# Kernel optimization log

Measured on AMD Instinct MI355X. Metric: run time of the kernel, lower is better.

The kernel has to match this reference:

```python
import jax, jax.numpy as jnp
import numpy as np

NEG_SLOPE = 0.2

def gatv2_layer(x, src, dst, Wl, bl, Wr, br, att, bias, N, concat):
    # Wl/Wr: [F_in, H*C]; att: [H, C]
    H, C = att.shape
    xl = (x @ Wl + bl).reshape(-1, H, C)  # source transform [N,H,C]
    xr = (x @ Wr + br).reshape(-1, H, C)  # target transform [N,H,C]
    e = jax.nn.leaky_relu(xl[src] + xr[dst], NEG_SLOPE)          # [E,H,C]
    logits = jnp.einsum('ehc,hc->eh', e, att)                    # [E,H]
    m = jax.ops.segment_max(logits, dst, num_segments=N)         # [N,H]
    p = jnp.exp(logits - m[dst])
    s = jax.ops.segment_sum(p, dst, num_segments=N)              # [N,H]
    alpha = p / s[dst]                                           # [E,H] softmax per dst
    out = jax.ops.segment_sum(alpha[:, :, None] * xl[src], dst, num_segments=N)  # [N,H,C]
    out = out.reshape(N, H * C) if concat else out.mean(axis=1)
    return out + bias


def setup_inputs() -> dict:
    key = jax.random.key(0)
    N, E, F_in = 50000, 500000, 58
    ks = jax.random.split(key, 16)
    s = 0.1
    inp = {
        'x': jax.random.normal(ks[0], (N, F_in), jnp.float32),
        'edge_index': jax.random.randint(ks[1], (2, E), 0, N, jnp.int64),
        'Wl1': jax.random.normal(ks[2], (F_in, 256), jnp.float32) * s,
        'bl1': jnp.zeros((256,), jnp.float32),
        'Wr1': jax.random.normal(ks[3], (F_in, 256), jnp.float32) * s,
        'br1': jnp.zeros((256,), jnp.float32),
        'att1': jax.random.normal(ks[4], (4, 64), jnp.float32) * s,
        'bias1': jnp.zeros((256,), jnp.float32),
        'Wl2': jax.random.normal(ks[5], (256, 256), jnp.float32) * s,
        'bl2': jnp.zeros((256,), jnp.float32),
        'Wr2': jax.random.normal(ks[6], (256, 256), jnp.float32) * s,
        'br2': jnp.zeros((256,), jnp.float32),
        'att2': jax.random.normal(ks[7], (4, 64), jnp.float32) * s,
        'bias2': jnp.zeros((256,), jnp.float32),
        'Wl3': jax.random.normal(ks[8], (256, 6), jnp.float32) * s,
        'bl3': jnp.zeros((6,), jnp.float32),
        'Wr3': jax.random.normal(ks[9], (256, 6), jnp.float32) * s,
        'br3': jnp.zeros((6,), jnp.float32),
        'att3': jax.random.normal(ks[10], (6, 1), jnp.float32) * s,
        'bias3': jnp.zeros((1,), jnp.float32),
    }
    return inp


def reference(x, edge_index, Wl1, bl1, Wr1, br1, att1, bias1,
              Wl2, bl2, Wr2, br2, att2, bias2,
              Wl3, bl3, Wr3, br3, att3, bias3):
    N = x.shape[0]
    loop = jnp.arange(N, dtype=edge_index.dtype)
    src = jnp.concatenate([edge_index[0], loop])  # self-loops (PyG default)
    dst = jnp.concatenate([edge_index[1], loop])
    h = jax.nn.elu(gatv2_layer(x, src, dst, Wl1, bl1, Wr1, br1, att1, bias1, N, True))
    h = jax.nn.elu(gatv2_layer(h, src, dst, Wl2, bl2, Wr2, br2, att2, bias2, N, True))
    out = gatv2_layer(h, src, dst, Wl3, bl3, Wr3, br3, att3, bias3, N, False)
    return out  # [N, 1]
```

## Files before the change

### kernel.cpp

```cpp
#include <hip/hip_runtime.h>
#include <math.h>

#define NEG_SLOPE 0.2f
#define LOG2E 1.4426950408889634f

typedef __attribute__((ext_vector_type(2))) _Float16 h2;
typedef __attribute__((ext_vector_type(4))) _Float16 h4;
typedef __attribute__((ext_vector_type(8))) _Float16 f16x8;
typedef __attribute__((ext_vector_type(4))) float f32x4;

typedef const __attribute__((address_space(1))) unsigned int* gu32p;
typedef __attribute__((address_space(3))) unsigned int* lu32p;

#define GLD16(g, l) __builtin_amdgcn_global_load_lds((gu32p)(g), (lu32p)(l), 16, 0, 0)

template<int CTRL>
__device__ __forceinline__ float dpp_add_f32(float x) {
    int y = __builtin_amdgcn_update_dpp(0, __float_as_int(x), CTRL, 0xF, 0xF, true);
    return x + __int_as_float(y);
}
__device__ __forceinline__ float rowsum16(float x) {
    x = dpp_add_f32<0xB1>(x);
    x = dpp_add_f32<0x4E>(x);
    x = dpp_add_f32<0x124>(x);
    x = dpp_add_f32<0x128>(x);
    return x;
}


__global__ __launch_bounds__(256) void k_scan_block(const int* __restrict__ cnt,
                                                    int* __restrict__ out,
                                                    int* __restrict__ bsums, int n) {
    __shared__ int tmp[256];
    int t = threadIdx.x;
    int i = blockIdx.x * 256 + t;
    int v = (i < n) ? cnt[i] : 0;
    tmp[t] = v;
    __syncthreads();
    for (int d = 1; d < 256; d <<= 1) {
        int add = (t >= d) ? tmp[t - d] : 0;
        __syncthreads();
        tmp[t] += add;
        __syncthreads();
    }
    if (i < n) out[i] = tmp[t] - v;
    if (t == 255) bsums[blockIdx.x] = tmp[t];
}

__global__ __launch_bounds__(256) void k_scan_bsums(int* bsums, int nb) {
    __shared__ int tmp[256];
    int t = threadIdx.x;
    int v = (t < nb) ? bsums[t] : 0;
    tmp[t] = v;
    __syncthreads();
    for (int d = 1; d < 256; d <<= 1) {
        int add = (t >= d) ? tmp[t - d] : 0;
        __syncthreads();
        tmp[t] += add;
        __syncthreads();
    }
    if (t < nb) bsums[t] = tmp[t] - v;
}

__global__ __launch_bounds__(256) void k_scan_add(int* __restrict__ out,
                                                  const int* __restrict__ bsums,
                                                  int* __restrict__ cursor,
                                                  int n, int total) {
    int i = blockIdx.x * 256 + threadIdx.x;
    if (i < n) {
        int v = out[i] + bsums[blockIdx.x];
        out[i] = v;
        cursor[i] = v;
    }
    if (i == 0) out[n] = total;
}

__global__ __launch_bounds__(256) void k_scatter(const int* __restrict__ ei, int E, int Et,
                                                 int* __restrict__ cursor,
                                                 int* __restrict__ src_sorted) {
    int e = blockIdx.x * 256 + threadIdx.x;
    if (e < Et) {
        int s, d;
        if (e < E) { s = ei[e]; d = ei[E + e]; } else { s = d = e - E; }
        int pos = atomicAdd(&cursor[d], 1);
        src_sorted[pos] = s;
    }
}


__global__ __launch_bounds__(256) void k_prep(
        const int* __restrict__ ei, int E, int Et, int* __restrict__ cnt,
        const float* __restrict__ x, _Float16* __restrict__ xb, int N, int F,
        const float* __restrict__ Wl1, const float* __restrict__ Wr1,
        const float* __restrict__ Wl2, const float* __restrict__ Wr2,
        const float* __restrict__ Wl3, const float* __restrict__ Wr3,
        _Float16* __restrict__ wtl1, _Float16* __restrict__ wtr1,
        _Float16* __restrict__ wtl2, _Float16* __restrict__ wtr2,
        _Float16* __restrict__ w3t, int gEt, int gX) {
    const int b = blockIdx.x;
    if (b < gEt) {
        int e = b * 256 + threadIdx.x;
        if (e < Et) {
            int d = (e < E) ? ei[E + e] : (e - E);
            atomicAdd(&cnt[d], 1);
        }
    } else if (b < gEt + gX) {
        int i = (b - gEt) * 256 + threadIdx.x;
        if (i < (N << 6)) {
            int n = i >> 6, k = i & 63;
            xb[i] = (_Float16)(k < F ? x[n * F + k] : 0.0f);
        }
    } else {
        int i = (b - gEt - gX) * 256 + threadIdx.x;
        if (i < 32768) {
            const float* W = (i < 16384) ? Wl1 : Wr1;
            _Float16* O = (i < 16384) ? wtl1 : wtr1;
            int loc = i & 16383;
            int n = loc >> 6, k = loc & 63;
            O[loc] = (_Float16)(k < F ? W[k * 256 + n] : 0.0f);
        } else if (i < 163840) {
            int seg = i - 32768;
            const float* W = (seg < 65536) ? Wl2 : Wr2;
            _Float16* O = (seg < 65536) ? wtl2 : wtr2;
            int loc = seg & 65535;
            int n = loc >> 8, k = loc & 255;
            O[loc] = (_Float16)W[k * 256 + n];
        } else if (i < 167936) {
            int loc = i - 163840;
            int j = loc >> 8, k = loc & 255;
            float v = (j < 6) ? Wl3[k * 6 + j] : ((j < 12) ? Wr3[k * 6 + (j - 6)] : 0.0f);
            w3t[loc] = (_Float16)v;
        }
    }
}


__global__ __launch_bounds__(256) void k_gemm_pair_mfma(
        const _Float16* __restrict__ A, int M, int Kp,
        const _Float16* __restrict__ Btl, const _Float16* __restrict__ Btr,
        const float* __restrict__ bl, const float* __restrict__ br,
        _Float16* __restrict__ Cl, _Float16* __restrict__ Cr) {
    __shared__ _Float16 As[128 * 32];
    __shared__ _Float16 Bs[128 * 32];
    const int wv = threadIdx.x >> 6, lane = threadIdx.x & 63;
    const int wr = wv >> 1, wc = wv & 1;
    const int l15 = lane & 15, l4 = lane >> 4;
    const int row0 = blockIdx.x * 128;
    const int mat  = blockIdx.y >> 1;
    const int col0 = (blockIdx.y & 1) * 128;
    const _Float16* Bt = mat ? Btr : Btl;
    const float* bias  = mat ? br  : bl;
    _Float16* C        = mat ? Cr  : Cl;

    const int rl = lane >> 2;
    const int kq = (lane & 3) * 8;
    const _Float16* ga0 = A + (size_t)min(row0 + wv * 32 + rl,      M - 1) * Kp + kq;
    const _Float16* ga1 = A + (size_t)min(row0 + wv * 32 + 16 + rl, M - 1) * Kp + kq;
    const _Float16* gb0 = Bt + (size_t)(col0 + wv * 32 + rl) * Kp + kq;
    const _Float16* gb1 = Bt + (size_t)(col0 + wv * 32 + 16 + rl) * Kp + kq;
    _Float16* la0 = &As[(wv * 32) * 32];
    _Float16* la1 = &As[(wv * 32 + 16) * 32];
    _Float16* lb0 = &Bs[(wv * 32) * 32];
    _Float16* lb1 = &Bs[(wv * 32 + 16) * 32];

    f32x4 acc[4][4];
    #pragma unroll
    for (int a = 0; a < 4; a++)
        #pragma unroll
        for (int b = 0; b < 4; b++)
            acc[a][b] = (f32x4){0.f, 0.f, 0.f, 0.f};

    for (int k0 = 0; k0 < Kp; k0 += 32) {
        GLD16(ga0 + k0, la0);
        GLD16(ga1 + k0, la1);
        GLD16(gb0 + k0, lb0);
        GLD16(gb1 + k0, lb1);
        __syncthreads();
        f16x8 wf[4], xf[4];
        #pragma unroll
        for (int ct = 0; ct < 4; ct++)
            wf[ct] = *(const f16x8*)&Bs[(wc * 64 + ct * 16 + l15) * 32 + l4 * 8];
        #pragma unroll
        for (int nt = 0; nt < 4; nt++)
            xf[nt] = *(const f16x8*)&As[(wr * 64 + nt * 16 + l15) * 32 + l4 * 8];
        #pragma unroll
        for (int ct = 0; ct < 4; ct++)
            #pragma unroll
            for (int nt = 0; nt < 4; nt++)
                acc[ct][nt] = __builtin_amdgcn_mfma_f32_16x16x32_f16(
                    wf[ct], xf[nt], acc[ct][nt], 0, 0, 0);
        __syncthreads();
    }

    float4 bv[4];
    #pragma unroll
    for (int ct = 0; ct < 4; ct++)
        bv[ct] = *(const float4*)&bias[col0 + wc * 64 + ct * 16 + l4 * 4];
    #pragma unroll
    for (int nt = 0; nt < 4; nt++) {
        int node = row0 + wr * 64 + nt * 16 + l15;
        if (node < M) {
            #pragma unroll
            for (int ct = 0; ct < 4; ct++) {
                h4 hv = {(_Float16)(acc[ct][nt][0] + bv[ct].x),
                         (_Float16)(acc[ct][nt][1] + bv[ct].y),
                         (_Float16)(acc[ct][nt][2] + bv[ct].z),
                         (_Float16)(acc[ct][nt][3] + bv[ct].w)};
                *(h4*)&C[(size_t)node * 256 + col0 + wc * 64 + ct * 16 + l4 * 4] = hv;
            }
        }
    }
}


__global__ __launch_bounds__(256) void k_gemm3_mfma(
        const _Float16* __restrict__ h,
        const _Float16* __restrict__ W3t,
        const float* __restrict__ bl, const float* __restrict__ br,
        _Float16* __restrict__ l3, int N) {
    const int wave = threadIdx.x >> 6, lane = threadIdx.x & 63;
    const int l15 = lane & 15, l4 = lane >> 4;
    const int row0 = blockIdx.x * 64 + wave * 16;
    if (row0 >= N) return;

    f16x8 bfr[8];
    #pragma unroll
    for (int ks = 0; ks < 8; ks++)
        bfr[ks] = *(const f16x8*)&W3t[l15 * 256 + ks * 32 + l4 * 8];

    const int arow = min(row0 + l15, N - 1);
    const size_t abase = (size_t)arow * 256;
    f32x4 acc = (f32x4){0.f, 0.f, 0.f, 0.f};
    #pragma unroll
    for (int ks = 0; ks < 8; ks++) {
        f16x8 af = *(const f16x8*)&h[abase + ks * 32 + l4 * 8];
        acc = __builtin_amdgcn_mfma_f32_16x16x32_f16(af, bfr[ks], acc, 0, 0, 0);
    }
    const float bv = (l15 < 6) ? bl[l15] : ((l15 < 12) ? br[l15 - 6] : 0.0f);
    #pragma unroll
    for (int r = 0; r < 4; r++) {
        int gr = row0 + l4 * 4 + r;
        if (gr < N && l15 < 12)
            l3[(size_t)gr * 16 + l15] = (_Float16)(acc[r] + bv);
    }
}


__global__ __launch_bounds__(256) void k_agg256(const _Float16* __restrict__ xl,
                                                const _Float16* __restrict__ xr,
                                                const int* __restrict__ row_ptr,
                                                const int* __restrict__ src_sorted,
                                                const float* __restrict__ att,
                                                const float* __restrict__ bias,
                                                _Float16* __restrict__ h_out, int N) {
    const int wave = threadIdx.x >> 6;
    const int lane = threadIdx.x & 63;
    const int n = __builtin_amdgcn_readfirstlane(blockIdx.x * 4 + wave);
    if (n >= N) return;
    const int ci = lane * 4;
    const h4 xr4 = *(const h4*)&xr[(size_t)n * 256 + ci];
    const float4 at4 = *(const float4*)&att[ci];
    const h2 ata = {(_Float16)(at4.x * LOG2E), (_Float16)(at4.y * LOG2E)};
    const h2 atb = {(_Float16)(at4.z * LOG2E), (_Float16)(at4.w * LOG2E)};
    float a0 = 0.f, a1 = 0.f, a2 = 0.f, a3 = 0.f;
    float m = -INFINITY, s = 0.0f;
    const int beg = row_ptr[n], end = row_ptr[n + 1];
    const int rem = (end - beg) & 7;
    const int tb  = end - rem;

    h4 vt[7];
    #pragma unroll
    for (int e = 0; e < 7; e++) {
        if (e < rem) {
            int sv = src_sorted[tb + e];
            vt[e] = *(const h4*)&xl[(size_t)sv * 256 + ci];
        }
    }

    int j = beg;
    h4 v[8], vn[8];
    bool has = (j + 8 <= tb);
    if (has) {
        #pragma unroll
        for (int e = 0; e < 8; e++) {
            int sv = src_sorted[j + e];
            v[e] = *(const h4*)&xl[(size_t)sv * 256 + ci];
        }
    }
    while (has) {
        const int jn = j + 8;
        const bool hasN = (jn + 8 <= tb);
        if (hasN) {
            #pragma unroll
            for (int e = 0; e < 8; e++) {
                int sv = src_sorted[jn + e];
                vn[e] = *(const h4*)&xl[(size_t)sv * 256 + ci];
            }
        }
        float lg[8];
        #pragma unroll
        for (int e = 0; e < 8; e++) {
            h4 t = v[e] + xr4;
            h4 lk = __builtin_elementwise_max(t, t * (_Float16)NEG_SLOPE);
            h2 lo = __builtin_shufflevector(lk, lk, 0, 1);
            h2 hi = __builtin_shufflevector(lk, lk, 2, 3);
            lg[e] = __builtin_amdgcn_fdot2(lo, ata,
                        __builtin_amdgcn_fdot2(hi, atb, 0.0f, false), false);
        }
        #pragma unroll
        for (int e = 0; e < 8; e++) lg[e] = rowsum16(lg[e]);
        float bm = fmaxf(fmaxf(fmaxf(lg[0], lg[1]), fmaxf(lg[2], lg[3])),
                         fmaxf(fmaxf(lg[4], lg[5]), fmaxf(lg[6], lg[7])));
        float nm = fmaxf(m, bm);
        float sc = __builtin_amdgcn_exp2f(m - nm);
        a0 *= sc; a1 *= sc; a2 *= sc; a3 *= sc;
        float ps = 0.f;
        #pragma unroll
        for (int e = 0; e < 8; e++) {
            float p = __builtin_amdgcn_exp2f(lg[e] - nm);
            ps += p;
            a0 = fmaf(p, (float)v[e].x, a0);
            a1 = fmaf(p, (float)v[e].y, a1);
            a2 = fmaf(p, (float)v[e].z, a2);
            a3 = fmaf(p, (float)v[e].w, a3);
        }
        s = s * sc + ps;
        m = nm;
        if (hasN) {
            #pragma unroll
            for (int e = 0; e < 8; e++) v[e] = vn[e];
        }
        j = jn;
        has = hasN;
    }

    if (rem) {
        float lg[7];
        #pragma unroll
        for (int e = 0; e < 7; e++) {
            if (e < rem) {
                h4 t = vt[e] + xr4;
                h4 lk = __builtin_elementwise_max(t, t * (_Float16)NEG_SLOPE);
                h2 lo = __builtin_shufflevector(lk, lk, 0, 1);
                h2 hi = __builtin_shufflevector(lk, lk, 2, 3);
                float d = __builtin_amdgcn_fdot2(lo, ata,
                              __builtin_amdgcn_fdot2(hi, atb, 0.0f, false), false);
                lg[e] = rowsum16(d);
            }
        }
        float bm = -INFINITY;
        #pragma unroll
        for (int e = 0; e < 7; e++)
            if (e < rem) bm = fmaxf(bm, lg[e]);
        float nm = fmaxf(m, bm);
        float sc = __builtin_amdgcn_exp2f(m - nm);
        a0 *= sc; a1 *= sc; a2 *= sc; a3 *= sc;
        float ps = 0.f;
        #pragma unroll
        for (int e = 0; e < 7; e++) {
            if (e < rem) {
                float p = __builtin_amdgcn_exp2f(lg[e] - nm);
                ps += p;
                a0 = fmaf(p, (float)vt[e].x, a0);
                a1 = fmaf(p, (float)vt[e].y, a1);
                a2 = fmaf(p, (float)vt[e].z, a2);
                a3 = fmaf(p, (float)vt[e].w, a3);
            }
        }
        s = s * sc + ps;
        m = nm;
    }

    const float inv = 1.0f / s;
    const float4 bv = *(const float4*)&bias[ci];
    float o0 = a0 * inv + bv.x;
    float o1 = a1 * inv + bv.y;
    float o2 = a2 * inv + bv.z;
    float o3 = a3 * inv + bv.w;
    o0 = o0 > 0.f ? o0 : (__expf(o0) - 1.f);
    o1 = o1 > 0.f ? o1 : (__expf(o1) - 1.f);
    o2 = o2 > 0.f ? o2 : (__expf(o2) - 1.f);
    o3 = o3 > 0.f ? o3 : (__expf(o3) - 1.f);
    h4 hv = {(_Float16)o0, (_Float16)o1, (_Float16)o2, (_Float16)o3};
    *(h4*)&h_out[(size_t)n * 256 + ci] = hv;
}


__global__ __launch_bounds__(256) void k_agg3(const _Float16* __restrict__ l3,
                                              const int* __restrict__ row_ptr,
                                              const int* __restrict__ src_sorted,
                                              const float* __restrict__ att3,
                                              const float* __restrict__ bias3,
                                              float* __restrict__ out, int N) {
    int n = blockIdx.x * 256 + threadIdx.x;
    if (n >= N) return;
    const h4* pn = (const h4*)&l3[(size_t)n * 16];
    h4 q1 = pn[1], q2 = pn[2];
    float xrv[6];
    xrv[0] = (float)q1.z; xrv[1] = (float)q1.w;
    xrv[2] = (float)q2.x; xrv[3] = (float)q2.y;
    xrv[4] = (float)q2.z; xrv[5] = (float)q2.w;
    float attv[6], m[6], s[6], acc[6];
    #pragma unroll
    for (int k = 0; k < 6; k++) {
        attv[k] = att3[k] * LOG2E;
        m[k] = -INFINITY; s[k] = 0.0f; acc[k] = 0.0f;
    }
    const int beg = row_ptr[n], end = row_ptr[n + 1];
    for (int j = beg; j < end; j += 8) {
        f16x8 u[8];
        #pragma unroll
        for (int e = 0; e < 8; e++) {
            int idx = j + e;
            idx = idx < end ? idx : end - 1;
            int sv = src_sorted[idx];
            u[e] = *(const f16x8*)&l3[(size_t)sv * 16];
        }
        #pragma unroll
        for (int e = 0; e < 8; e++) {
            const bool valid = (j + e) < end;
            float xlv[6];
            #pragma unroll
            for (int k = 0; k < 6; k++) xlv[k] = (float)u[e][k];
            #pragma unroll
            for (int k = 0; k < 6; k++) {
                float tt = xlv[k] + xrv[k];
                float lr = fmaxf(tt, NEG_SLOPE * tt);
                float logit = valid ? (attv[k] * lr) : -INFINITY;
                float nm = fmaxf(m[k], logit);
                float sc = __builtin_amdgcn_exp2f(m[k] - nm);
                float p  = __builtin_amdgcn_exp2f(logit - nm);
                acc[k] = acc[k] * sc + p * xlv[k];
                s[k]   = s[k] * sc + p;
                m[k]   = nm;
            }
        }
    }
    float o = 0.0f;
    #pragma unroll
    for (int k = 0; k < 6; k++) o += acc[k] / s[k];
    out[n] = o * (1.0f / 6.0f) + bias3[0];
}


extern "C" void kernel_launch(void* const* d_in, const int* in_sizes, int n_in,
                              void* d_out, int out_size, void* d_ws, size_t ws_size,
                              hipStream_t stream) {
    const float* x    = (const float*)d_in[0];
    const int*   ei   = (const int*)  d_in[1];
    const float* Wl1  = (const float*)d_in[2];
    const float* bl1  = (const float*)d_in[3];
    const float* Wr1  = (const float*)d_in[4];
    const float* br1  = (const float*)d_in[5];
    const float* att1 = (const float*)d_in[6];
    const float* bias1= (const float*)d_in[7];
    const float* Wl2  = (const float*)d_in[8];
    const float* bl2  = (const float*)d_in[9];
    const float* Wr2  = (const float*)d_in[10];
    const float* br2  = (const float*)d_in[11];
    const float* att2 = (const float*)d_in[12];
    const float* bias2= (const float*)d_in[13];
    const float* Wl3  = (const float*)d_in[14];
    const float* bl3  = (const float*)d_in[15];
    const float* Wr3  = (const float*)d_in[16];
    const float* br3  = (const float*)d_in[17];
    const float* att3 = (const float*)d_in[18];
    const float* bias3= (const float*)d_in[19];

    const int F  = in_sizes[2] / 256;
    const int N  = in_sizes[0] / F;
    const int E  = in_sizes[1] / 2;
    const int Et = E + N;

    char* ws = (char*)d_ws;
    size_t off = 0;
    auto carve = [&](size_t bytes) -> char* {
        char* p = ws + off;
        off = (off + bytes + 255) & ~(size_t)255;
        return p;
    };
    _Float16* xb   = (_Float16*)carve((size_t)N * 64 * 2);
    _Float16* xlb  = (_Float16*)carve((size_t)N * 256 * 2);
    _Float16* xrb  = (_Float16*)carve((size_t)N * 256 * 2);
    _Float16* hb   = (_Float16*)carve((size_t)N * 256 * 2);
    _Float16* wtl1 = (_Float16*)carve(256 * 64 * 2);
    _Float16* wtr1 = (_Float16*)carve(256 * 64 * 2);
    _Float16* wtl2 = (_Float16*)carve(256 * 256 * 2);
    _Float16* wtr2 = (_Float16*)carve(256 * 256 * 2);
    _Float16* w3t  = (_Float16*)carve(16 * 256 * 2);
    _Float16* l3   = (_Float16*)carve((size_t)N * 16 * 2);
    int* cnt        = (int*)carve((size_t)N * 4);
    int* row_ptr    = (int*)carve((size_t)(N + 1) * 4);
    int* cursor     = (int*)carve((size_t)N * 4);
    int* src_sorted = (int*)carve((size_t)Et * 4);
    int* bsums      = (int*)carve(1024 * 4);

    const int gN  = (N + 255) / 256;
    const int gEt = (Et + 255) / 256;
    const int gX  = ((N << 6) + 255) / 256;
    const int gW  = (N + 3) / 4;

    hipMemsetAsync(cnt, 0, (size_t)N * 4, stream);
    k_prep<<<gEt + gX + 656, 256, 0, stream>>>(ei, E, Et, cnt, x, xb, N, F,
                                               Wl1, Wr1, Wl2, Wr2, Wl3, Wr3,
                                               wtl1, wtr1, wtl2, wtr2, w3t, gEt, gX);

    k_scan_block<<<gN, 256, 0, stream>>>(cnt, row_ptr, bsums, N);
    k_scan_bsums<<<1, 256, 0, stream>>>(bsums, gN);
    k_scan_add<<<gN, 256, 0, stream>>>(row_ptr, bsums, cursor, N, Et);
    k_scatter<<<gEt, 256, 0, stream>>>(ei, E, Et, cursor, src_sorted);

    dim3 gemm_grid((N + 127) / 128, 4);

    k_gemm_pair_mfma<<<gemm_grid, 256, 0, stream>>>(xb, N, 64, wtl1, wtr1, bl1, br1, xlb, xrb);
    k_agg256<<<gW, 256, 0, stream>>>(xlb, xrb, row_ptr, src_sorted, att1, bias1, hb, N);

    k_gemm_pair_mfma<<<gemm_grid, 256, 0, stream>>>(hb, N, 256, wtl2, wtr2, bl2, br2, xlb, xrb);
    k_agg256<<<gW, 256, 0, stream>>>(xlb, xrb, row_ptr, src_sorted, att2, bias2, hb, N);

    k_gemm3_mfma<<<(N + 63) / 64, 256, 0, stream>>>(hb, w3t, bl3, br3, l3, N);
    k_agg3<<<(N + 255) / 256, 256, 0, stream>>>(l3, row_ptr, src_sorted, att3, bias3,
                                                (float*)d_out, N);
}
```

Measured before the change: 332.2 us.

## Fuse scan stages, merge edge scatter into first GEMM, widen GEMM tile

After: 324.2 us. 2.4% less time.

```diff
diff --git a/kernel.cpp b/kernel.cpp
--- a/kernel.cpp
+++ b/kernel.cpp
@@ -47,7 +47,10 @@
     if (t == 255) bsums[blockIdx.x] = tmp[t];
 }
 
-__global__ __launch_bounds__(256) void k_scan_bsums(int* bsums, int nb) {
+__global__ __launch_bounds__(256) void k_scan_add(int* __restrict__ out,
+                                                  const int* __restrict__ bsums,
+                                                  int* __restrict__ cursor,
+                                                  int n, int total, int nb) {
     __shared__ int tmp[256];
     int t = threadIdx.x;
     int v = (t < nb) ? bsums[t] : 0;
@@ -59,32 +62,14 @@
         tmp[t] += add;
         __syncthreads();
     }
-    if (t < nb) bsums[t] = tmp[t] - v;
-}
-
-__global__ __launch_bounds__(256) void k_scan_add(int* __restrict__ out,
-                                                  const int* __restrict__ bsums,
-                                                  int* __restrict__ cursor,
-                                                  int n, int total) {
-    int i = blockIdx.x * 256 + threadIdx.x;
+    int boff = tmp[blockIdx.x] - bsums[blockIdx.x];
+    int i = blockIdx.x * 256 + t;
     if (i < n) {
-        int v = out[i] + bsums[blockIdx.x];
-        out[i] = v;
-        cursor[i] = v;
+        int vv = out[i] + boff;
+        out[i] = vv;
+        cursor[i] = vv;
     }
     if (i == 0) out[n] = total;
-}
-
-__global__ __launch_bounds__(256) void k_scatter(const int* __restrict__ ei, int E, int Et,
-                                                 int* __restrict__ cursor,
-                                                 int* __restrict__ src_sorted) {
-    int e = blockIdx.x * 256 + threadIdx.x;
-    if (e < Et) {
-        int s, d;
-        if (e < E) { s = ei[e]; d = ei[E + e]; } else { s = d = e - E; }
-        int pos = atomicAdd(&cursor[d], 1);
-        src_sorted[pos] = s;
-    }
 }
 
 
@@ -135,33 +120,46 @@
 }
 
 
-__global__ __launch_bounds__(256) void k_gemm_pair_mfma(
+__global__ __launch_bounds__(512) void k_gemm_pair_mfma(
         const _Float16* __restrict__ A, int M, int Kp,
         const _Float16* __restrict__ Btl, const _Float16* __restrict__ Btr,
         const float* __restrict__ bl, const float* __restrict__ br,
-        _Float16* __restrict__ Cl, _Float16* __restrict__ Cr) {
+        _Float16* __restrict__ Cl, _Float16* __restrict__ Cr,
+        const int* __restrict__ ei, int E, int Et,
+        int* __restrict__ cursor, int* __restrict__ src_sorted,
+        int sB, int gX) {
     __shared__ _Float16 As[128 * 32];
-    __shared__ _Float16 Bs[128 * 32];
-    const int wv = threadIdx.x >> 6, lane = threadIdx.x & 63;
-    const int wr = wv >> 1, wc = wv & 1;
+    __shared__ _Float16 Bs[256 * 32];
+    if (blockIdx.x < sB) {
+        int e = blockIdx.x * 512 + threadIdx.x;
+        if (e < Et) {
+            int s, d;
+            if (e < E) { s = ei[e]; d = ei[E + e]; } else { s = d = e - E; }
+            int pos = atomicAdd(&cursor[d], 1);
+            src_sorted[pos] = s;
+        }
+        return;
+    }
+    const int gb = blockIdx.x - sB;
+    const int mat = gb >= gX;
+    const int bx  = mat ? gb - gX : gb;
+    const int tid = threadIdx.x;
+    const int wv = tid >> 6, lane = tid & 63;
+    const int wr = wv >> 2, wc = wv & 3;
     const int l15 = lane & 15, l4 = lane >> 4;
-    const int row0 = blockIdx.x * 128;
-    const int mat  = blockIdx.y >> 1;
-    const int col0 = (blockIdx.y & 1) * 128;
+    const int row0 = bx * 128;
     const _Float16* Bt = mat ? Btr : Btl;
     const float* bias  = mat ? br  : bl;
     _Float16* C        = mat ? Cr  : Cl;
 
-    const int rl = lane >> 2;
-    const int kq = (lane & 3) * 8;
-    const _Float16* ga0 = A + (size_t)min(row0 + wv * 32 + rl,      M - 1) * Kp + kq;
-    const _Float16* ga1 = A + (size_t)min(row0 + wv * 32 + 16 + rl, M - 1) * Kp + kq;
-    const _Float16* gb0 = Bt + (size_t)(col0 + wv * 32 + rl) * Kp + kq;
-    const _Float16* gb1 = Bt + (size_t)(col0 + wv * 32 + 16 + rl) * Kp + kq;
-    _Float16* la0 = &As[(wv * 32) * 32];
-    _Float16* la1 = &As[(wv * 32 + 16) * 32];
-    _Float16* lb0 = &Bs[(wv * 32) * 32];
-    _Float16* lb1 = &Bs[(wv * 32 + 16) * 32];
+    const int sr = tid >> 2;
+    const int sk = (tid & 3) * 8;
+    const _Float16* gA  = A  + (size_t)min(row0 + sr, M - 1) * Kp + sk;
+    const _Float16* gB0 = Bt + (size_t)sr * Kp + sk;
+    const _Float16* gB1 = Bt + (size_t)(sr + 128) * Kp + sk;
+    _Float16* lA  = &As[(wv * 16) * 32];
+    _Float16* lB0 = &Bs[(wv * 16) * 32];
+    _Float16* lB1 = &Bs[(wv * 16 + 128) * 32];
 
     f32x4 acc[4][4];
     #pragma unroll
@@ -171,10 +169,9 @@
             acc[a][b] = (f32x4){0.f, 0.f, 0.f, 0.f};
 
     for (int k0 = 0; k0 < Kp; k0 += 32) {
-        GLD16(ga0 + k0, la0);
-        GLD16(ga1 + k0, la1);
-        GLD16(gb0 + k0, lb0);
-        GLD16(gb1 + k0, lb1);
+        GLD16(gA + k0, lA);
+        GLD16(gB0 + k0, lB0);
+        GLD16(gB1 + k0, lB1);
         __syncthreads();
         f16x8 wf[4], xf[4];
         #pragma unroll
@@ -195,7 +192,7 @@
     float4 bv[4];
     #pragma unroll
     for (int ct = 0; ct < 4; ct++)
-        bv[ct] = *(const float4*)&bias[col0 + wc * 64 + ct * 16 + l4 * 4];
+        bv[ct] = *(const float4*)&bias[wc * 64 + ct * 16 + l4 * 4];
     #pragma unroll
     for (int nt = 0; nt < 4; nt++) {
         int node = row0 + wr * 64 + nt * 16 + l15;
@@ -206,7 +203,7 @@
                          (_Float16)(acc[ct][nt][1] + bv[ct].y),
                          (_Float16)(acc[ct][nt][2] + bv[ct].z),
                          (_Float16)(acc[ct][nt][3] + bv[ct].w)};
-                *(h4*)&C[(size_t)node * 256 + col0 + wc * 64 + ct * 16 + l4 * 4] = hv;
+                *(h4*)&C[(size_t)node * 256 + wc * 64 + ct * 16 + l4 * 4] = hv;
             }
         }
     }
@@ -499,6 +496,8 @@
     const int gEt = (Et + 255) / 256;
     const int gX  = ((N << 6) + 255) / 256;
     const int gW  = (N + 3) / 4;
+    const int gx1 = (N + 127) / 128;
+    const int sB  = (Et + 511) / 512;
 
     hipMemsetAsync(cnt, 0, (size_t)N * 4, stream);
     k_prep<<<gEt + gX + 656, 256, 0, stream>>>(ei, E, Et, cnt, x, xb, N, F,
@@ -506,16 +505,16 @@
                                                wtl1, wtr1, wtl2, wtr2, w3t, gEt, gX);
 
     k_scan_block<<<gN, 256, 0, stream>>>(cnt, row_ptr, bsums, N);
-    k_scan_bsums<<<1, 256, 0, stream>>>(bsums, gN);
-    k_scan_add<<<gN, 256, 0, stream>>>(row_ptr, bsums, cursor, N, Et);
-    k_scatter<<<gEt, 256, 0, stream>>>(ei, E, Et, cursor, src_sorted);
-
-    dim3 gemm_grid((N + 127) / 128, 4);
-
-    k_gemm_pair_mfma<<<gemm_grid, 256, 0, stream>>>(xb, N, 64, wtl1, wtr1, bl1, br1, xlb, xrb);
+    k_scan_add<<<gN, 256, 0, stream>>>(row_ptr, bsums, cursor, N, Et, gN);
+
+    k_gemm_pair_mfma<<<sB + 2 * gx1, 512, 0, stream>>>(
+        xb, N, 64, wtl1, wtr1, bl1, br1, xlb, xrb,
+        ei, E, Et, cursor, src_sorted, sB, gx1);
     k_agg256<<<gW, 256, 0, stream>>>(xlb, xrb, row_ptr, src_sorted, att1, bias1, hb, N);
 
-    k_gemm_pair_mfma<<<gemm_grid, 256, 0, stream>>>(hb, N, 256, wtl2, wtr2, bl2, br2, xlb, xrb);
+    k_gemm_pair_mfma<<<2 * gx1, 512, 0, stream>>>(
+        hb, N, 256, wtl2, wtr2, bl2, br2, xlb, xrb,
+        ei, E, Et, cursor, src_sorted, 0, gx1);
     k_agg256<<<gW, 256, 0, stream>>>(xlb, xrb, row_ptr, src_sorted, att2, bias2, hb, N);
 
     k_gemm3_mfma<<<(N + 63) / 64, 256, 0, stream>>>(hb, w3t, bl3, br3, l3, N);
```
